# Optimization experiments

Hardware: AMD Instinct MI355X
Metric: run time of the kernel (lower is better)

## Reference

```python
import jax, jax.numpy as jnp
from jax import lax
import numpy as np

# ---- config (repo globals, scaled to a 112x112 feature map of a 448 image) ----
IMG, FEAT = 448, 112
PSTRIDE = IMG // FEAT  # 4 pixels per feature cell
RATIOS = [(16, 16), (12, 20), (20, 12),
          (24, 24), (20, 28), (28, 20),
          (32, 32), (24, 40), (40, 24), (28, 40), (40, 28), (28, 36), (36, 28)]
GROUPS = [(0, 3), (3, 6), (6, 13)]   # ratio groups per NMS scale
N_LIST = [2, 3, 2]
IOU_THRESHS = [0.25, 0.25, 0.25]
BATCH = 256
WINDOW_NUMS = [(FEAT - rh + 1) * (FEAT - rw + 1) for rh, rw in RATIOS]
TOTAL = sum(WINDOW_NUMS)             # 96981
PROPOSALN = sum(N_LIST)              # 7


def _coordinates():
    # Mirrors ComputeCoordinate: box = [x0,y0,x1,y1] in pixels, lefttop clipped to 0.
    parts = []
    for rh, rw in RATIOS:
        nr, nc = FEAT - rh + 1, FEAT - rw + 1
        xi = np.repeat(np.arange(nr), nc).astype(np.float32)
        yi = np.tile(np.arange(nc), nr).astype(np.float32)
        x0 = xi * PSTRIDE - 1.0
        y0 = yi * PSTRIDE - 1.0
        x1 = x0 + rh * PSTRIDE
        y1 = y0 + rw * PSTRIDE
        x0 = np.maximum(x0, 0.0)
        y0 = np.maximum(y0, 0.0)
        parts.append(np.stack([x0, y0, x1, y1], 1))
    return np.concatenate(parts, 0).astype(np.float32)  # (TOTAL, 4)


def setup_inputs() -> dict:
    key = jax.random.key(0)
    x = jax.random.normal(key, (BATCH, 1, FEAT, FEAT), jnp.float32)
    coords = jnp.asarray(_coordinates())
    return {"x": x, "coords": coords, "proposalN": PROPOSALN}


def _nms(scores, coords, n_pick, thresh):
    # Greedy NMS: repeatedly take best-scoring alive window, suppress IoU > thresh.
    # If everything is suppressed before n_pick picks, repeat the last pick (repo behavior).
    areas = (coords[:, 2] - coords[:, 0] + 1.0) * (coords[:, 3] - coords[:, 1] + 1.0)

    def step(state, _):
        alive, last = state
        any_alive = jnp.any(alive)
        idx = jnp.where(any_alive,
                        jnp.argmax(jnp.where(alive, scores, -jnp.inf)).astype(jnp.int32),
                        last)
        box = coords[idx]
        lt = jnp.maximum(coords[:, :2], box[:2])
        rb = jnp.minimum(coords[:, 2:], box[2:])
        w = rb[:, 0] - lt[:, 0] + 1.0
        h = rb[:, 1] - lt[:, 1] + 1.0
        inter = jnp.where((w < 0) | (h < 0), 0.0, w * h)
        iou = inter / (areas + areas[idx] - inter)
        keep = (alive & (iou <= thresh)).at[idx].set(False)
        return (jnp.where(any_alive, keep, alive), idx), idx

    init = (jnp.ones(scores.shape[0], bool), jnp.int32(0))
    return lax.scan(step, init, None, length=n_pick)[1]  # (n_pick,) int32


def _forward(x, coords):
    B = x.shape[0]
    # multiscale sliding-window average scores (AvgPool2d, stride 1, VALID)
    avgs = [lax.reduce_window(x, 0.0, lax.add, (1, 1, rh, rw), (1, 1, 1, 1), 'VALID')
            .reshape(B, -1) / float(rh * rw) for rh, rw in RATIOS]
    all_scores = jnp.concatenate(avgs, 1)  # (B, TOTAL)

    idx_parts = []
    for j, (g0, g1) in enumerate(GROUPS):
        s0 = int(sum(WINDOW_NUMS[:g0]))
        s1 = int(sum(WINDOW_NUMS[:g1]))
        cd = coords[s0:s1]
        nms_j = lambda s, cd=cd, j=j: _nms(s, cd, N_LIST[j], IOU_THRESHS[j])
        picks = jax.vmap(nms_j)(all_scores[:, s0:s1])  # (B, N_LIST[j])
        idx_parts.append(picks + s0)
    proposalN_indices = jnp.concatenate(idx_parts, 1)  # (B, PROPOSALN)
    proposalN_windows_scores = jnp.take_along_axis(all_scores, proposalN_indices, 1)
    window_scores = all_scores  # reshape(batch, -1) of all_scores
    return proposalN_indices, proposalN_windows_scores, window_scores


def reference(x, coords, proposalN):
    assert proposalN == PROPOSALN
    return _forward(x, coords)
```

## Files before the change

kernel.cpp:

```cpp
#include <hip/hip_runtime.h>
#include <math.h>
#include <limits.h>

namespace {
constexpr int kFeat = 112;
constexpr int kBatch = 256;
constexpr int kTotal = 96981;
constexpr int kStride = 116;
constexpr int kNT = 512;
constexpr int kRH[13] = {16,12,20,24,20,28,32,24,40,28,40,28,36};
constexpr int kRW[13] = {16,20,12,24,28,20,32,40,24,40,28,36,28};
constexpr int kOff[13] = {0,9409,18802,28195,36116,44021,51926,58487,64984,71481,77686,83891,90436};
}

struct NmsShared {
  float rs[kNT / 64];
  int   ri[kNT / 64];
  float shS; int shI;
  float pX0[3], pY0[3], pX1[3], pY1[3], pA[3];
};

__device__ __forceinline__ void block_argmax(float s, int i, NmsShared* ns) {
  __syncthreads();
#pragma unroll
  for (int off = 32; off > 0; off >>= 1) {
    const float s2 = __shfl_down(s, off, 64);
    const int   i2 = __shfl_down(i, off, 64);
    if (s2 > s || (s2 == s && i2 < i)) { s = s2; i = i2; }
  }
  const int wave = threadIdx.x >> 6;
  if ((threadIdx.x & 63) == 0) { ns->rs[wave] = s; ns->ri[wave] = i; }
  __syncthreads();
  if (threadIdx.x == 0) {
    float bs = ns->rs[0]; int bi = ns->ri[0];
#pragma unroll
    for (int w = 1; w < kNT / 64; ++w)
      if (ns->rs[w] > bs || (ns->rs[w] == bs && ns->ri[w] < bi)) { bs = ns->rs[w]; bi = ns->ri[w]; }
    ns->shS = bs; ns->shI = bi;
  }
  __syncthreads();
}

__device__ void build_sat(const float* __restrict__ xb, float* __restrict__ sat) {
  const int tid = threadIdx.x;
  for (int j = tid; j < kStride; j += kNT) sat[j] = 0.f;
  for (int r = tid; r < 113; r += kNT) sat[r * kStride] = 0.f;
  const float4* x4 = (const float4*)xb;
  for (int i = tid; i < (kFeat * kFeat) / 4; i += kNT) {
    const float4 v = x4[i];
    const int r = i / (kFeat / 4);
    const int c = (i - r * (kFeat / 4)) * 4;
    float* dst = sat + (r + 1) * kStride + c + 1;
    dst[0] = v.x; dst[1] = v.y; dst[2] = v.z; dst[3] = v.w;
  }
  __syncthreads();
  const int wave = tid >> 6, lane = tid & 63;
  for (int r = 1 + wave; r <= kFeat; r += kNT / 64) {
    float* row = sat + r * kStride;
    float v = row[1 + lane];
#pragma unroll
    for (int d = 1; d < 64; d <<= 1) { const float u = __shfl_up(v, d, 64); if (lane >= d) v += u; }
    row[1 + lane] = v;
    const float tot = __shfl(v, 63, 64);
    const int c = 65 + lane;
    float w = (c <= kFeat) ? row[c] : 0.f;
#pragma unroll
    for (int d = 1; d < 64; d <<= 1) { const float u = __shfl_up(w, d, 64); if (lane >= d) w += u; }
    if (c <= kFeat) row[c] = w + tot;
  }
  __syncthreads();
  const int seg = tid / kFeat;
  const int col = tid - seg * kFeat + 1;
  if (tid < 4 * kFeat) {
    const int r0 = seg * 28 + 1;
    float s = 0.f;
    for (int r = r0; r < r0 + 28; ++r) { s += sat[r * kStride + col]; sat[r * kStride + col] = s; }
  }
  __syncthreads();
  float off = 0.f;
  if (tid < 4 * kFeat && seg > 0) {
#pragma unroll
    for (int s2 = 1; s2 <= 3; ++s2)
      if (s2 <= seg) off += sat[(28 * s2) * kStride + col];
  }
  __syncthreads();
  if (tid < 4 * kFeat && seg > 0) {
    const int r0 = seg * 28 + 1;
    for (int r = r0; r < r0 + 28; ++r) sat[r * kStride + col] += off;
  }
  __syncthreads();
}

template<int RB, int RE>
__device__ __forceinline__ void pick_store(NmsShared* ns, int k, int slot,
                                           float* __restrict__ out_idx,
                                           float* __restrict__ out_sc, int b) {
  if (threadIdx.x == 0) {
    const int pi = ns->shI;
#pragma unroll
    for (int rr = RB; rr < RE; ++rr) {
      const int nr = kFeat - kRH[rr] + 1, nc = kFeat - kRW[rr] + 1;
      if (pi >= kOff[rr] && pi < kOff[rr] + nr * nc) {
        const int l = pi - kOff[rr];
        const int xi = l / nc, yi = l - xi * nc;
        const float x0u = xi * 4.0f - 1.0f, y0u = yi * 4.0f - 1.0f;
        const float x1 = x0u + kRH[rr] * 4.0f, y1 = y0u + kRW[rr] * 4.0f;
        const float x0 = fmaxf(x0u, 0.0f), y0 = fmaxf(y0u, 0.0f);
        ns->pX0[k] = x0; ns->pY0[k] = y0; ns->pX1[k] = x1; ns->pY1[k] = y1;
        ns->pA[k] = (x1 - x0 + 1.0f) * (y1 - y0 + 1.0f);
      }
    }
    out_idx[b * 7 + slot + k] = (float)pi;
    out_sc [b * 7 + slot + k] = ns->shS;
  }
  __syncthreads();
}

template<int RB, int RE, int NP, int SLOT>
__device__ void run_group(const float* __restrict__ sat, NmsShared* ns,
                          float* __restrict__ wb,
                          float* __restrict__ out_idx, float* __restrict__ out_sc, int b) {
  const int tid = threadIdx.x;
  float best = -INFINITY; int bi = INT_MAX;

#pragma unroll
  for (int rr = RB; rr < RE; ++rr) {
    const int rh = kRH[rr], rw = kRW[rr];
    const int nr = kFeat - rh + 1, nc = kFeat - rw + 1;
    const int nqy = (nc + 3) >> 2;
    const float inv = 1.0f / (float)(rh * rw);
    for (int q = tid; q < nr * nqy; q += kNT) {
      const int xi = q / nqy, qy = q - xi * nqy;
      const int yi0 = qy << 2;
      const float* u = sat + xi * kStride;
      const float* d = u + rh * kStride;
      const float4 U0 = *(const float4*)(u + yi0);
      const float4 U1 = *(const float4*)(u + yi0 + rw);
      const float4 D0 = *(const float4*)(d + yi0);
      const float4 D1 = *(const float4*)(d + yi0 + rw);
      const float s0 = (D1.x - U1.x - D0.x + U0.x) * inv;
      const float s1 = (D1.y - U1.y - D0.y + U0.y) * inv;
      const float s2 = (D1.z - U1.z - D0.z + U0.z) * inv;
      const float s3 = (D1.w - U1.w - D0.w + U0.w) * inv;
      const int gi0 = kOff[rr] + xi * nc + yi0;
      float* w = wb + gi0;
      const int rem = nc - yi0;
      w[0] = s0; if (s0 > best) { best = s0; bi = gi0; }
      if (rem > 1) { w[1] = s1; if (s1 > best) { best = s1; bi = gi0 + 1; } }
      if (rem > 2) { w[2] = s2; if (s2 > best) { best = s2; bi = gi0 + 2; } }
      if (rem > 3) { w[3] = s3; if (s3 > best) { best = s3; bi = gi0 + 3; } }
    }
  }

  block_argmax(best, bi, ns);
  pick_store<RB, RE>(ns, 0, SLOT, out_idx, out_sc, b);

  for (int k = 1; k < NP; ++k) {
    float px0[NP], py0[NP], px1[NP], py1[NP], pa[NP];
#pragma unroll
    for (int p = 0; p < NP; ++p) {
      if (p < k) { px0[p] = ns->pX0[p]; py0[p] = ns->pY0[p]; px1[p] = ns->pX1[p];
                   py1[p] = ns->pY1[p]; pa[p] = ns->pA[p]; }
    }
    best = -INFINITY; bi = INT_MAX;
#pragma unroll
    for (int rr = RB; rr < RE; ++rr) {
      const int rh = kRH[rr], rw = kRW[rr];
      const int nr = kFeat - rh + 1, nc = kFeat - rw + 1;
      const int nqy = (nc + 3) >> 2;
      const float inv = 1.0f / (float)(rh * rw);
      for (int q = tid; q < nr * nqy; q += kNT) {
        const int xi = q / nqy, qy = q - xi * nqy;
        const int yi0 = qy << 2;
        const float* u = sat + xi * kStride;
        const float* d = u + rh * kStride;
        const float4 U0 = *(const float4*)(u + yi0);
        const float4 U1 = *(const float4*)(u + yi0 + rw);
        const float4 D0 = *(const float4*)(d + yi0);
        const float4 D1 = *(const float4*)(d + yi0 + rw);
        float s4[4];
        s4[0] = (D1.x - U1.x - D0.x + U0.x) * inv;
        s4[1] = (D1.y - U1.y - D0.y + U0.y) * inv;
        s4[2] = (D1.z - U1.z - D0.z + U0.z) * inv;
        s4[3] = (D1.w - U1.w - D0.w + U0.w) * inv;
        const float X0u = xi * 4.0f - 1.0f;
        const float X1 = X0u + rh * 4.0f;
        const float X0 = fmaxf(X0u, 0.0f);
        const float Ax = X1 - X0 + 1.0f;
        float wx[NP];
#pragma unroll
        for (int p = 0; p < NP; ++p)
          if (p < k) wx[p] = fminf(X1, px1[p]) - fmaxf(X0, px0[p]) + 1.0f;
        const int gi0 = kOff[rr] + xi * nc + yi0;
        const int rem = nc - yi0;
#pragma unroll
        for (int j = 0; j < 4; ++j) {
          if (j >= rem) break;
          const float Y0u = (yi0 + j) * 4.0f - 1.0f;
          const float Y1 = Y0u + rw * 4.0f;
          const float Y0 = fmaxf(Y0u, 0.0f);
          const float A = Ax * (Y1 - Y0 + 1.0f);
          bool alive = true;
#pragma unroll
          for (int p = 0; p < NP; ++p) {
            if (p >= k) break;
            const float hy = fminf(Y1, py1[p]) - fmaxf(Y0, py0[p]) + 1.0f;
            const bool sup = (wx[p] >= 0.0f) & (hy >= 0.0f) &
                             (5.0f * wx[p] * hy > A + pa[p]);
            alive &= !sup;
          }
          if (alive && s4[j] > best) { best = s4[j]; bi = gi0 + j; }
        }
      }
    }
    block_argmax(best, bi, ns);
    pick_store<RB, RE>(ns, k, SLOT, out_idx, out_sc, b);
  }
}

__global__ __launch_bounds__(kNT, 6) void appm_fused(const float* __restrict__ x,
                                                     float* __restrict__ win,
                                                     float* __restrict__ out_idx,
                                                     float* __restrict__ out_sc) {
  __shared__ __align__(16) float sat[113 * kStride];
  __shared__ NmsShared ns;
  const int b = blockIdx.x / 3;
  const int t = blockIdx.x % 3;

  build_sat(x + (size_t)b * kFeat * kFeat, sat);

  float* wb = win + (size_t)b * kTotal;
  if (t == 0)       run_group<0, 3, 2, 0>(sat, &ns, wb, out_idx, out_sc, b);
  else if (t == 1)  run_group<3, 6, 3, 2>(sat, &ns, wb, out_idx, out_sc, b);
  else              run_group<6, 13, 2, 5>(sat, &ns, wb, out_idx, out_sc, b);
}

extern "C" void kernel_launch(void* const* d_in, const int* in_sizes, int n_in,
                              void* d_out, int out_size, void* d_ws, size_t ws_size,
                              hipStream_t stream) {
  const float* x = (const float*)d_in[0];
  float* out     = (float*)d_out;
  float* out_idx = out;
  float* out_sc  = out + kBatch * 7;
  float* win     = out + 2 * kBatch * 7;

  appm_fused<<<kBatch * 3, kNT, 0, stream>>>(x, win, out_idx, out_sc);
}
```

Baseline: 165.6 us.

## Cache per-thread top-4 candidates to skip NMS rescans of window scores

During the first scoring pass, each thread now keeps a sorted top-4 list of its own window scores and indices instead of a single best. In later NMS picks the thread first checks those cached candidates against the previous picks and uses the first one that is not suppressed. It only recomputes its windows from the summed-area table when all four cached candidates are suppressed. This removes most of the repeated full scans, at the cost of insertion work and extra registers in the first pass, which may reduce occupancy under the launch bounds.

```diff
diff --git a/kernel.cpp b/kernel.cpp
--- a/kernel.cpp
+++ b/kernel.cpp
@@ -8,6 +8,7 @@
 constexpr int kTotal = 96981;
 constexpr int kStride = 116;
 constexpr int kNT = 512;
+constexpr int kL = 4;
 constexpr int kRH[13] = {16,12,20,24,20,28,32,24,40,28,40,28,36};
 constexpr int kRW[13] = {16,20,12,24,28,20,32,40,24,40,28,36,28};
 constexpr int kOff[13] = {0,9409,18802,28195,36116,44021,51926,58487,64984,71481,77686,83891,90436};
@@ -91,6 +92,41 @@
   __syncthreads();
 }
 
+__device__ __forceinline__ bool cand_better(float s, int i, float s2, int i2) {
+  return s > s2 || (s == s2 && i < i2);
+}
+
+__device__ __forceinline__ void topl_insert(float (&cs)[kL], int (&ci)[kL], float s, int i) {
+  if (!cand_better(s, i, cs[kL - 1], ci[kL - 1])) return;
+  cs[kL - 1] = s; ci[kL - 1] = i;
+#pragma unroll
+  for (int c = kL - 2; c >= 0; --c) {
+    if (cand_better(cs[c + 1], ci[c + 1], cs[c], ci[c])) {
+      const float ts = cs[c]; const int ti = ci[c];
+      cs[c] = cs[c + 1]; ci[c] = ci[c + 1];
+      cs[c + 1] = ts; ci[c + 1] = ti;
+    }
+  }
+}
+
+template<int RB, int RE>
+__device__ __forceinline__ void decode_geom(int pi, float& x0, float& y0,
+                                            float& x1, float& y1, float& a) {
+  x0 = 0.f; y0 = 0.f; x1 = 0.f; y1 = 0.f; a = 0.f;
+#pragma unroll
+  for (int rr = RB; rr < RE; ++rr) {
+    const int nr = kFeat - kRH[rr] + 1, nc = kFeat - kRW[rr] + 1;
+    if (pi >= kOff[rr] && pi < kOff[rr] + nr * nc) {
+      const int l = pi - kOff[rr];
+      const int xi = l / nc, yi = l - xi * nc;
+      const float x0u = xi * 4.0f - 1.0f, y0u = yi * 4.0f - 1.0f;
+      x1 = x0u + kRH[rr] * 4.0f; y1 = y0u + kRW[rr] * 4.0f;
+      x0 = fmaxf(x0u, 0.0f); y0 = fmaxf(y0u, 0.0f);
+      a = (x1 - x0 + 1.0f) * (y1 - y0 + 1.0f);
+    }
+  }
+}
+
 template<int RB, int RE>
 __device__ __forceinline__ void pick_store(NmsShared* ns, int k, int slot,
                                            float* __restrict__ out_idx,
@@ -121,7 +157,9 @@
                           float* __restrict__ wb,
                           float* __restrict__ out_idx, float* __restrict__ out_sc, int b) {
   const int tid = threadIdx.x;
-  float best = -INFINITY; int bi = INT_MAX;
+  float cs[kL]; int ci[kL];
+#pragma unroll
+  for (int c = 0; c < kL; ++c) { cs[c] = -INFINITY; ci[c] = INT_MAX; }
 
 #pragma unroll
   for (int rr = RB; rr < RE; ++rr) {
@@ -145,14 +183,14 @@
       const int gi0 = kOff[rr] + xi * nc + yi0;
       float* w = wb + gi0;
       const int rem = nc - yi0;
-      w[0] = s0; if (s0 > best) { best = s0; bi = gi0; }
-      if (rem > 1) { w[1] = s1; if (s1 > best) { best = s1; bi = gi0 + 1; } }
-      if (rem > 2) { w[2] = s2; if (s2 > best) { best = s2; bi = gi0 + 2; } }
-      if (rem > 3) { w[3] = s3; if (s3 > best) { best = s3; bi = gi0 + 3; } }
-    }
-  }
-
-  block_argmax(best, bi, ns);
+      w[0] = s0; topl_insert(cs, ci, s0, gi0);
+      if (rem > 1) { w[1] = s1; topl_insert(cs, ci, s1, gi0 + 1); }
+      if (rem > 2) { w[2] = s2; topl_insert(cs, ci, s2, gi0 + 2); }
+      if (rem > 3) { w[3] = s3; topl_insert(cs, ci, s3, gi0 + 3); }
+    }
+  }
+
+  block_argmax(cs[0], ci[0], ns);
   pick_store<RB, RE>(ns, 0, SLOT, out_idx, out_sc, b);
 
   for (int k = 1; k < NP; ++k) {
@@ -162,57 +200,79 @@
       if (p < k) { px0[p] = ns->pX0[p]; py0[p] = ns->pY0[p]; px1[p] = ns->pX1[p];
                    py1[p] = ns->pY1[p]; pa[p] = ns->pA[p]; }
     }
-    best = -INFINITY; bi = INT_MAX;
-#pragma unroll
-    for (int rr = RB; rr < RE; ++rr) {
-      const int rh = kRH[rr], rw = kRW[rr];
-      const int nr = kFeat - rh + 1, nc = kFeat - rw + 1;
-      const int nqy = (nc + 3) >> 2;
-      const float inv = 1.0f / (float)(rh * rw);
-      for (int q = tid; q < nr * nqy; q += kNT) {
-        const int xi = q / nqy, qy = q - xi * nqy;
-        const int yi0 = qy << 2;
-        const float* u = sat + xi * kStride;
-        const float* d = u + rh * kStride;
-        const float4 U0 = *(const float4*)(u + yi0);
-        const float4 U1 = *(const float4*)(u + yi0 + rw);
-        const float4 D0 = *(const float4*)(d + yi0);
-        const float4 D1 = *(const float4*)(d + yi0 + rw);
-        float s4[4];
-        s4[0] = (D1.x - U1.x - D0.x + U0.x) * inv;
-        s4[1] = (D1.y - U1.y - D0.y + U0.y) * inv;
-        s4[2] = (D1.z - U1.z - D0.z + U0.z) * inv;
-        s4[3] = (D1.w - U1.w - D0.w + U0.w) * inv;
-        const float X0u = xi * 4.0f - 1.0f;
-        const float X1 = X0u + rh * 4.0f;
-        const float X0 = fmaxf(X0u, 0.0f);
-        const float Ax = X1 - X0 + 1.0f;
-        float wx[NP];
-#pragma unroll
-        for (int p = 0; p < NP; ++p)
-          if (p < k) wx[p] = fminf(X1, px1[p]) - fmaxf(X0, px0[p]) + 1.0f;
-        const int gi0 = kOff[rr] + xi * nc + yi0;
-        const int rem = nc - yi0;
-#pragma unroll
-        for (int j = 0; j < 4; ++j) {
-          if (j >= rem) break;
-          const float Y0u = (yi0 + j) * 4.0f - 1.0f;
-          const float Y1 = Y0u + rw * 4.0f;
-          const float Y0 = fmaxf(Y0u, 0.0f);
-          const float A = Ax * (Y1 - Y0 + 1.0f);
-          bool alive = true;
-#pragma unroll
-          for (int p = 0; p < NP; ++p) {
-            if (p >= k) break;
-            const float hy = fminf(Y1, py1[p]) - fmaxf(Y0, py0[p]) + 1.0f;
-            const bool sup = (wx[p] >= 0.0f) & (hy >= 0.0f) &
-                             (5.0f * wx[p] * hy > A + pa[p]);
-            alive &= !sup;
+
+    float best = -INFINITY; int bi = INT_MAX; bool found = false;
+#pragma unroll
+    for (int c = 0; c < kL; ++c) {
+      if (!found) {
+        float x0, y0, x1, y1, a;
+        decode_geom<RB, RE>(ci[c], x0, y0, x1, y1, a);
+        bool sup = false;
+#pragma unroll
+        for (int p = 0; p < NP; ++p) {
+          if (p < k) {
+            const float wx = fminf(x1, px1[p]) - fmaxf(x0, px0[p]) + 1.0f;
+            const float hy = fminf(y1, py1[p]) - fmaxf(y0, py0[p]) + 1.0f;
+            sup = sup | ((wx >= 0.0f) & (hy >= 0.0f) & (5.0f * wx * hy > a + pa[p]));
           }
-          if (alive && s4[j] > best) { best = s4[j]; bi = gi0 + j; }
+        }
+        if (!sup) { best = cs[c]; bi = ci[c]; found = true; }
+      }
+    }
+
+    if (!found) {
+#pragma unroll
+      for (int rr = RB; rr < RE; ++rr) {
+        const int rh = kRH[rr], rw = kRW[rr];
+        const int nr = kFeat - rh + 1, nc = kFeat - rw + 1;
+        const int nqy = (nc + 3) >> 2;
+        const float inv = 1.0f / (float)(rh * rw);
+        for (int q = tid; q < nr * nqy; q += kNT) {
+          const int xi = q / nqy, qy = q - xi * nqy;
+          const int yi0 = qy << 2;
+          const float* u = sat + xi * kStride;
+          const float* d = u + rh * kStride;
+          const float4 U0 = *(const float4*)(u + yi0);
+          const float4 U1 = *(const float4*)(u + yi0 + rw);
+          const float4 D0 = *(const float4*)(d + yi0);
+          const float4 D1 = *(const float4*)(d + yi0 + rw);
+          float s4[4];
+          s4[0] = (D1.x - U1.x - D0.x + U0.x) * inv;
+          s4[1] = (D1.y - U1.y - D0.y + U0.y) * inv;
+          s4[2] = (D1.z - U1.z - D0.z + U0.z) * inv;
+          s4[3] = (D1.w - U1.w - D0.w + U0.w) * inv;
+          const float X0u = xi * 4.0f - 1.0f;
+          const float X1 = X0u + rh * 4.0f;
+          const float X0 = fmaxf(X0u, 0.0f);
+          const float Ax = X1 - X0 + 1.0f;
+          float wxp[NP];
+#pragma unroll
+          for (int p = 0; p < NP; ++p)
+            if (p < k) wxp[p] = fminf(X1, px1[p]) - fmaxf(X0, px0[p]) + 1.0f;
+          const int gi0 = kOff[rr] + xi * nc + yi0;
+          const int rem = nc - yi0;
+#pragma unroll
+          for (int j = 0; j < 4; ++j) {
+            if (j >= rem) break;
+            const float Y0u = (yi0 + j) * 4.0f - 1.0f;
+            const float Y1 = Y0u + rw * 4.0f;
+            const float Y0 = fmaxf(Y0u, 0.0f);
+            const float A = Ax * (Y1 - Y0 + 1.0f);
+            bool alive = true;
+#pragma unroll
+            for (int p = 0; p < NP; ++p) {
+              if (p >= k) break;
+              const float hy = fminf(Y1, py1[p]) - fmaxf(Y0, py0[p]) + 1.0f;
+              const bool sup = (wxp[p] >= 0.0f) & (hy >= 0.0f) &
+                               (5.0f * wxp[p] * hy > A + pa[p]);
+              alive &= !sup;
+            }
+            if (alive && s4[j] > best) { best = s4[j]; bi = gi0 + j; }
+          }
         }
       }
     }
+
     block_argmax(best, bi, ns);
     pick_store<RB, RE>(ns, k, SLOT, out_idx, out_sc, b);
   }
```

Result: slower. 184.0 us (+11.1%).

## Cache per-wave bucket maxima and rescan only suppressed buckets in NMS

Applied to the files above, without the earlier changes.

In the first pass each wave records the maximum score and index of its 64-entry chunk into a shared table. Later NMS rounds re-evaluate only the chunks whose current best box is suppressed by the newest pick, instead of rescanning every window. This avoids the full recompute-and-suppress sweep on each pick, at the cost of an extra table, more irregular per-wave work and added code complexity.

```diff
diff --git a/kernel.cpp b/kernel.cpp
--- a/kernel.cpp
+++ b/kernel.cpp
@@ -1,6 +1,7 @@
 #include <hip/hip_runtime.h>
 #include <math.h>
 #include <limits.h>
+#include <float.h>
 
 namespace {
 constexpr int kFeat = 112;
@@ -11,6 +12,16 @@
 constexpr int kRH[13] = {16,12,20,24,20,28,32,24,40,28,40,28,36};
 constexpr int kRW[13] = {16,20,12,24,28,20,32,40,24,40,28,36,28};
 constexpr int kOff[13] = {0,9409,18802,28195,36116,44021,51926,58487,64984,71481,77686,83891,90436};
+constexpr int kNQY[13] = {25,24,26,23,22,24,21,19,23,19,22,20,22};
+constexpr int kNQ[13]  = {2425,2424,2418,2047,2046,2040,1701,1691,1679,1615,1606,1700,1694};
+constexpr int kNB[13]  = {38,38,38,32,32,32,27,27,27,26,26,27,27};
+constexpr int kNBMax = 187;
+
+constexpr int nb_sum(int RB, int RE) {
+  int s = 0;
+  for (int r = RB; r < RE; ++r) s += kNB[r];
+  return s;
+}
 }
 
 struct NmsShared {
@@ -92,24 +103,32 @@
 }
 
 template<int RB, int RE>
+__device__ __forceinline__ void decode_geom(int pi, float& x0, float& y0,
+                                            float& x1, float& y1, float& a) {
+  x0 = 0.f; y0 = 0.f; x1 = 0.f; y1 = 0.f; a = 0.f;
+#pragma unroll
+  for (int rr = RB; rr < RE; ++rr) {
+    const int nr = kFeat - kRH[rr] + 1, nc = kFeat - kRW[rr] + 1;
+    if (pi >= kOff[rr] && pi < kOff[rr] + nr * nc) {
+      const int l = pi - kOff[rr];
+      const int xi = l / nc, yi = l - xi * nc;
+      const float x0u = xi * 4.0f - 1.0f, y0u = yi * 4.0f - 1.0f;
+      x1 = x0u + kRH[rr] * 4.0f; y1 = y0u + kRW[rr] * 4.0f;
+      x0 = fmaxf(x0u, 0.0f); y0 = fmaxf(y0u, 0.0f);
+      a = (x1 - x0 + 1.0f) * (y1 - y0 + 1.0f);
+    }
+  }
+}
+
+template<int RB, int RE>
 __device__ __forceinline__ void pick_store(NmsShared* ns, int k, int slot,
                                            float* __restrict__ out_idx,
                                            float* __restrict__ out_sc, int b) {
   if (threadIdx.x == 0) {
     const int pi = ns->shI;
-#pragma unroll
-    for (int rr = RB; rr < RE; ++rr) {
-      const int nr = kFeat - kRH[rr] + 1, nc = kFeat - kRW[rr] + 1;
-      if (pi >= kOff[rr] && pi < kOff[rr] + nr * nc) {
-        const int l = pi - kOff[rr];
-        const int xi = l / nc, yi = l - xi * nc;
-        const float x0u = xi * 4.0f - 1.0f, y0u = yi * 4.0f - 1.0f;
-        const float x1 = x0u + kRH[rr] * 4.0f, y1 = y0u + kRW[rr] * 4.0f;
-        const float x0 = fmaxf(x0u, 0.0f), y0 = fmaxf(y0u, 0.0f);
-        ns->pX0[k] = x0; ns->pY0[k] = y0; ns->pX1[k] = x1; ns->pY1[k] = y1;
-        ns->pA[k] = (x1 - x0 + 1.0f) * (y1 - y0 + 1.0f);
-      }
-    }
+    float x0, y0, x1, y1, a;
+    decode_geom<RB, RE>(pi, x0, y0, x1, y1, a);
+    ns->pX0[k] = x0; ns->pY0[k] = y0; ns->pX1[k] = x1; ns->pY1[k] = y1; ns->pA[k] = a;
     out_idx[b * 7 + slot + k] = (float)pi;
     out_sc [b * 7 + slot + k] = ns->shS;
   }
@@ -118,19 +137,27 @@
 
 template<int RB, int RE, int NP, int SLOT>
 __device__ void run_group(const float* __restrict__ sat, NmsShared* ns,
+                          float* __restrict__ tabS, int* __restrict__ tabI,
                           float* __restrict__ wb,
                           float* __restrict__ out_idx, float* __restrict__ out_sc, int b) {
+  constexpr int NBtot = nb_sum(RB, RE);
   const int tid = threadIdx.x;
-  float best = -INFINITY; int bi = INT_MAX;
-
+  const int lane = tid & 63;
+  const int wave = tid >> 6;
+
+  int eb = 0;
 #pragma unroll
   for (int rr = RB; rr < RE; ++rr) {
     const int rh = kRH[rr], rw = kRW[rr];
-    const int nr = kFeat - rh + 1, nc = kFeat - rw + 1;
-    const int nqy = (nc + 3) >> 2;
+    const int nc = kFeat - rw + 1;
+    const int nqy = kNQY[rr];
+    const int NQ = kNQ[rr];
     const float inv = 1.0f / (float)(rh * rw);
-    for (int q = tid; q < nr * nqy; q += kNT) {
-      const int xi = q / nqy, qy = q - xi * nqy;
+    for (int qb = (tid & ~63); qb < NQ; qb += kNT) {
+      const int q = qb + lane;
+      const bool act = q < NQ;
+      const int qc = act ? q : NQ - 1;
+      const int xi = qc / nqy, qy = qc - xi * nqy;
       const int yi0 = qy << 2;
       const float* u = sat + xi * kStride;
       const float* d = u + rh * kStride;
@@ -143,77 +170,116 @@
       const float s2 = (D1.z - U1.z - D0.z + U0.z) * inv;
       const float s3 = (D1.w - U1.w - D0.w + U0.w) * inv;
       const int gi0 = kOff[rr] + xi * nc + yi0;
-      float* w = wb + gi0;
       const int rem = nc - yi0;
-      w[0] = s0; if (s0 > best) { best = s0; bi = gi0; }
-      if (rem > 1) { w[1] = s1; if (s1 > best) { best = s1; bi = gi0 + 1; } }
-      if (rem > 2) { w[2] = s2; if (s2 > best) { best = s2; bi = gi0 + 2; } }
-      if (rem > 3) { w[3] = s3; if (s3 > best) { best = s3; bi = gi0 + 3; } }
+      float bs = -INFINITY; int bgi = INT_MAX;
+      if (act) {
+        float* w = wb + gi0;
+        w[0] = s0; bs = s0; bgi = gi0;
+        if (rem > 1) { w[1] = s1; if (s1 > bs) { bs = s1; bgi = gi0 + 1; } }
+        if (rem > 2) { w[2] = s2; if (s2 > bs) { bs = s2; bgi = gi0 + 2; } }
+        if (rem > 3) { w[3] = s3; if (s3 > bs) { bs = s3; bgi = gi0 + 3; } }
+      }
+      float wm = bs;
+#pragma unroll
+      for (int off = 32; off > 0; off >>= 1) wm = fmaxf(wm, __shfl_down(wm, off, 64));
+      wm = __shfl(wm, 0, 64);
+      const unsigned long long bal = __ballot(bs == wm);
+      if (lane == __ffsll(bal) - 1) { tabS[eb + (qb >> 6)] = wm; tabI[eb + (qb >> 6)] = bgi; }
     }
-  }
-
-  block_argmax(best, bi, ns);
+    eb += kNB[rr];
+  }
+  __syncthreads();
+
+  {
+    const float s = (tid < NBtot) ? tabS[tid] : -INFINITY;
+    const int   i = (tid < NBtot) ? tabI[tid] : INT_MAX;
+    block_argmax(s, i, ns);
+  }
   pick_store<RB, RE>(ns, 0, SLOT, out_idx, out_sc, b);
 
   for (int k = 1; k < NP; ++k) {
-    float px0[NP], py0[NP], px1[NP], py1[NP], pa[NP];
-#pragma unroll
-    for (int p = 0; p < NP; ++p) {
-      if (p < k) { px0[p] = ns->pX0[p]; py0[p] = ns->pY0[p]; px1[p] = ns->pX1[p];
-                   py1[p] = ns->pY1[p]; pa[p] = ns->pA[p]; }
-    }
-    best = -INFINITY; bi = INT_MAX;
-#pragma unroll
-    for (int rr = RB; rr < RE; ++rr) {
-      const int rh = kRH[rr], rw = kRW[rr];
-      const int nr = kFeat - rh + 1, nc = kFeat - rw + 1;
-      const int nqy = (nc + 3) >> 2;
-      const float inv = 1.0f / (float)(rh * rw);
-      for (int q = tid; q < nr * nqy; q += kNT) {
-        const int xi = q / nqy, qy = q - xi * nqy;
-        const int yi0 = qy << 2;
-        const float* u = sat + xi * kStride;
-        const float* d = u + rh * kStride;
-        const float4 U0 = *(const float4*)(u + yi0);
-        const float4 U1 = *(const float4*)(u + yi0 + rw);
-        const float4 D0 = *(const float4*)(d + yi0);
-        const float4 D1 = *(const float4*)(d + yi0 + rw);
-        float s4[4];
-        s4[0] = (D1.x - U1.x - D0.x + U0.x) * inv;
-        s4[1] = (D1.y - U1.y - D0.y + U0.y) * inv;
-        s4[2] = (D1.z - U1.z - D0.z + U0.z) * inv;
-        s4[3] = (D1.w - U1.w - D0.w + U0.w) * inv;
-        const float X0u = xi * 4.0f - 1.0f;
-        const float X1 = X0u + rh * 4.0f;
-        const float X0 = fmaxf(X0u, 0.0f);
-        const float Ax = X1 - X0 + 1.0f;
-        float wx[NP];
-#pragma unroll
-        for (int p = 0; p < NP; ++p)
-          if (p < k) wx[p] = fminf(X1, px1[p]) - fmaxf(X0, px0[p]) + 1.0f;
-        const int gi0 = kOff[rr] + xi * nc + yi0;
-        const int rem = nc - yi0;
-#pragma unroll
-        for (int j = 0; j < 4; ++j) {
-          if (j >= rem) break;
-          const float Y0u = (yi0 + j) * 4.0f - 1.0f;
-          const float Y1 = Y0u + rw * 4.0f;
-          const float Y0 = fmaxf(Y0u, 0.0f);
-          const float A = Ax * (Y1 - Y0 + 1.0f);
-          bool alive = true;
-#pragma unroll
-          for (int p = 0; p < NP; ++p) {
-            if (p >= k) break;
-            const float hy = fminf(Y1, py1[p]) - fmaxf(Y0, py0[p]) + 1.0f;
-            const bool sup = (wx[p] >= 0.0f) & (hy >= 0.0f) &
-                             (5.0f * wx[p] * hy > A + pa[p]);
-            alive &= !sup;
+    const float nx0 = ns->pX0[k-1], ny0 = ns->pY0[k-1];
+    const float nx1 = ns->pX1[k-1], ny1 = ns->pY1[k-1], na = ns->pA[k-1];
+    for (int e = wave; e < NBtot; e += kNT / 64) {
+      const float es = tabS[e];
+      if (es == -INFINITY) continue;
+      float x0, y0, x1, y1, a;
+      decode_geom<RB, RE>(tabI[e], x0, y0, x1, y1, a);
+      const float twx = fminf(x1, nx1) - fmaxf(x0, nx0) + 1.0f;
+      const float thy = fminf(y1, ny1) - fmaxf(y0, ny0) + 1.0f;
+      const bool sup = (twx >= 0.0f) & (thy >= 0.0f) & (5.0f * twx * thy > a + na);
+      if (!sup) continue;
+      int ebase = 0;
+#pragma unroll
+      for (int rr = RB; rr < RE; ++rr) {
+        if (e >= ebase && e < ebase + kNB[rr]) {
+          const int rh = kRH[rr], rw = kRW[rr];
+          const int nc = kFeat - rw + 1;
+          const int nqy = kNQY[rr];
+          const int NQ = kNQ[rr];
+          const float inv = 1.0f / (float)(rh * rw);
+          const int q = ((e - ebase) << 6) + lane;
+          const bool act = q < NQ;
+          const int qc = act ? q : NQ - 1;
+          const int xi = qc / nqy, qy = qc - xi * nqy;
+          const int yi0 = qy << 2;
+          const float* u = sat + xi * kStride;
+          const float* d = u + rh * kStride;
+          const float4 U0 = *(const float4*)(u + yi0);
+          const float4 U1 = *(const float4*)(u + yi0 + rw);
+          const float4 D0 = *(const float4*)(d + yi0);
+          const float4 D1 = *(const float4*)(d + yi0 + rw);
+          float s4[4];
+          s4[0] = (D1.x - U1.x - D0.x + U0.x) * inv;
+          s4[1] = (D1.y - U1.y - D0.y + U0.y) * inv;
+          s4[2] = (D1.z - U1.z - D0.z + U0.z) * inv;
+          s4[3] = (D1.w - U1.w - D0.w + U0.w) * inv;
+          const float X0u = xi * 4.0f - 1.0f;
+          const float X1 = X0u + rh * 4.0f;
+          const float X0 = fmaxf(X0u, 0.0f);
+          const float Ax = X1 - X0 + 1.0f;
+          float wxp[NP > 1 ? NP - 1 : 1];
+#pragma unroll
+          for (int p = 0; p < NP - 1; ++p)
+            if (p < k) wxp[p] = fminf(X1, ns->pX1[p]) - fmaxf(X0, ns->pX0[p]) + 1.0f;
+          const int gi0 = kOff[rr] + xi * nc + yi0;
+          const int rem = nc - yi0;
+          float bs = -INFINITY; int bgi = INT_MAX;
+          if (act) {
+#pragma unroll
+            for (int j = 0; j < 4; ++j) {
+              if (j >= rem) break;
+              const float Y0u = (yi0 + j) * 4.0f - 1.0f;
+              const float Y1 = Y0u + rw * 4.0f;
+              const float Y0 = fmaxf(Y0u, 0.0f);
+              const float A = Ax * (Y1 - Y0 + 1.0f);
+              bool alive = true;
+#pragma unroll
+              for (int p = 0; p < NP - 1; ++p) {
+                if (p >= k) break;
+                const float hyp = fminf(Y1, ns->pY1[p]) - fmaxf(Y0, ns->pY0[p]) + 1.0f;
+                alive &= !((wxp[p] >= 0.0f) & (hyp >= 0.0f) &
+                           (5.0f * wxp[p] * hyp > A + ns->pA[p]));
+              }
+              if (alive && s4[j] > bs) { bs = s4[j]; bgi = gi0 + j; }
+            }
           }
-          if (alive && s4[j] > best) { best = s4[j]; bi = gi0 + j; }
+          float wm = bs;
+#pragma unroll
+          for (int off = 32; off > 0; off >>= 1) wm = fmaxf(wm, __shfl_down(wm, off, 64));
+          wm = __shfl(wm, 0, 64);
+          const unsigned long long bal = __ballot(bs == wm);
+          if (lane == __ffsll(bal) - 1) { tabS[e] = wm; tabI[e] = bgi; }
         }
+        ebase += kNB[rr];
       }
     }
-    block_argmax(best, bi, ns);
+    __syncthreads();
+    {
+      const float s = (tid < NBtot) ? tabS[tid] : -INFINITY;
+      const int   i = (tid < NBtot) ? tabI[tid] : INT_MAX;
+      block_argmax(s, i, ns);
+    }
     pick_store<RB, RE>(ns, k, SLOT, out_idx, out_sc, b);
   }
 }
@@ -224,15 +290,17 @@
                                                      float* __restrict__ out_sc) {
   __shared__ __align__(16) float sat[113 * kStride];
   __shared__ NmsShared ns;
+  __shared__ float tabS[kNBMax];
+  __shared__ int   tabI[kNBMax];
   const int b = blockIdx.x / 3;
   const int t = blockIdx.x % 3;
 
   build_sat(x + (size_t)b * kFeat * kFeat, sat);
 
   float* wb = win + (size_t)b * kTotal;
-  if (t == 0)       run_group<0, 3, 2, 0>(sat, &ns, wb, out_idx, out_sc, b);
-  else if (t == 1)  run_group<3, 6, 3, 2>(sat, &ns, wb, out_idx, out_sc, b);
-  else              run_group<6, 13, 2, 5>(sat, &ns, wb, out_idx, out_sc, b);
+  if (t == 0)       run_group<0, 3, 2, 0>(sat, &ns, tabS, tabI, wb, out_idx, out_sc, b);
+  else if (t == 1)  run_group<3, 6, 3, 2>(sat, &ns, tabS, tabI, wb, out_idx, out_sc, b);
+  else              run_group<6, 13, 2, 5>(sat, &ns, tabS, tabI, wb, out_idx, out_sc, b);
 }
 
 extern "C" void kernel_launch(void* const* d_in, const int* in_sizes, int n_in,
```

After: 198.9 us. 1.2x slower.
